# Performance work log

Hardware: AMD Instinct MI355X
Metric: run time of the kernel (lower is better)

## Reference

```python
import jax, jax.numpy as jnp
import numpy as np

B, C, H, W = 8, 3, 720, 1280


def setup_inputs() -> dict:
    key = jax.random.key(0)
    k0, k1 = jax.random.split(key)
    im0 = jax.random.normal(k0, (B, C, H, W), dtype=jnp.float32)
    flow = jax.random.normal(k1, (B, H, W, 2), dtype=jnp.float32)
    return {"im0": im0, "flow": flow}


def reference(im0, flow):
    # Bilinear forward warp (interpolation_mode == 0).
    b, c, h, w = im0.shape
    gy, gx = jnp.meshgrid(jnp.arange(h, dtype=flow.dtype),
                          jnp.arange(w, dtype=flow.dtype), indexing="ij")
    x = gx[None] + flow[..., 0]  # [B,H,W] destination x
    y = gy[None] + flow[..., 1]  # [B,H,W] destination y

    x0 = jnp.floor(x)
    y0 = jnp.floor(y)
    wx1 = x - x0   # weight for x0+1
    wx0 = 1.0 - wx1
    wy1 = y - y0
    wy0 = 1.0 - wy1

    # source values: [B*H*W, C]
    vals = im0.transpose(0, 2, 3, 1).reshape(b * h * w, c)
    boff = (jnp.arange(b, dtype=jnp.int32) * (h * w))[:, None, None]
    out = jnp.zeros((b * h * w, c), dtype=im0.dtype)

    corners = ((x0, y0, wx0 * wy0),
               (x0 + 1.0, y0, wx1 * wy0),
               (x0, y0 + 1.0, wx0 * wy1),
               (x0 + 1.0, y0 + 1.0, wx1 * wy1))
    for xc, yc, wc in corners:
        xi = xc.astype(jnp.int32)
        yi = yc.astype(jnp.int32)
        valid = (xi >= 0) & (xi < w) & (yi >= 0) & (yi < h)
        xi = jnp.clip(xi, 0, w - 1)
        yi = jnp.clip(yi, 0, h - 1)
        idx = (boff + yi * w + xi).reshape(-1)           # [B*H*W]
        wt = jnp.where(valid, wc, 0.0).reshape(-1, 1)    # [B*H*W,1]
        out = out.at[idx].add(wt * vals)
    return out.reshape(b, h, w, c).transpose(0, 3, 1, 2)
```

## Files before the change

kernel.cpp:

```cpp
#include <hip/hip_runtime.h>
#include <hip/hip_fp16.h>

#define BB 8
#define CC 3
#define HH 720
#define WW 1280
#define PLANE (HH*WW)
#define NPIX (BB*HH*WW)

#define PXX 64
#define PYY 8
#define RAD 3
#define NBX (WW/PXX)
#define NBY (HH/PYY)
#define NBLK (BB*NBY*NBX)
#define WINX (PXX+2*RAD)
#define WINY (PYY+2*RAD)
#define NWIN (WINX*WINY)
#define CX 65
#define CY (PYY+1)
#define NCELL (CX*CY)
#define DEPTH 4
#define THREADS 512
#define NBATCH 2
#define OVF_CAP 64

#define OFF_FXY 0
#define OFF_V01 (NCELL*DEPTH)
#define OFF_V2  (2*NCELL*DEPTH)
#define OFF_CNT (2*NCELL*DEPTH + NCELL*DEPTH/2)
#define OFF_LOVF (OFF_CNT + NCELL)
#define LDS_DW  (OFF_LOVF + 1)

static __device__ __forceinline__ float h2f_lo(unsigned int u) {
    return __half2float(__ushort_as_half((unsigned short)(u & 0xffffu)));
}
static __device__ __forceinline__ float h2f_hi(unsigned int u) {
    return __half2float(__ushort_as_half((unsigned short)(u >> 16)));
}

__global__ __launch_bounds__(THREADS) void fw_gather(
    const float* __restrict__ im0,
    const float* __restrict__ flow,
    float* __restrict__ out,
    unsigned int* __restrict__ cnt_g,
    float* __restrict__ ovf_rec)
{
    __shared__ __align__(16) unsigned int lds[LDS_DW];
    unsigned int* FXY = lds + OFF_FXY;
    unsigned int* V01 = lds + OFF_V01;
    unsigned short* V2h = (unsigned short*)(lds + OFF_V2);
    unsigned int* CNT = lds + OFF_CNT;
    unsigned int* LOVF = lds + OFF_LOVF;

    const int phys = blockIdx.x;
    const int virt = (phys & 7) * (NBLK / 8) + (phys >> 3);
    const int b  = virt / (NBX * NBY);
    int r2 = virt - b * (NBX * NBY);
    const int by = r2 / NBX;
    const int bx = r2 - by * NBX;
    const int X0 = bx * PXX, Y0 = by * PYY;
    const int tid = threadIdx.x;

    float2 fv[NBATCH];
    float pv0[NBATCH], pv1[NBATCH], pv2[NBATCH];
    int pgx[NBATCH], pgy[NBATCH];
    bool pok[NBATCH];
#pragma unroll
    for (int t = 0; t < NBATCH; ++t) {
        int i = tid + t * THREADS;
        int wy = i / WINX;
        int wx = i - wy * WINX;
        int gx = X0 - RAD + wx;
        int gy = Y0 - RAD + wy;
        pok[t] = (i < NWIN) & (gx >= 0) & (gx < WW) & (gy >= 0) & (gy < HH);
        pgx[t] = gx; pgy[t] = gy;
        int cgx = min(max(gx, 0), WW - 1);
        int cgy = min(max(gy, 0), HH - 1);
        fv[t] = reinterpret_cast<const float2*>(flow)[(b * HH + cgy) * WW + cgx];
        int src = b * CC * PLANE + cgy * WW + cgx;
        pv0[t] = im0[src];
        pv1[t] = im0[src + PLANE];
        pv2[t] = im0[src + 2 * PLANE];
    }

    uint4* lds4 = reinterpret_cast<uint4*>(lds);
    for (int i = tid; i < LDS_DW / 4; i += THREADS)
        lds4[i] = make_uint4(0u, 0u, 0u, 0u);
    __syncthreads();

#pragma unroll
    for (int t = 0; t < NBATCH; ++t) {
        if (!pok[t]) continue;
        float2 f = fv[t];
        int gx = pgx[t], gy = pgy[t];
        bool reg = (f.x >= -(float)RAD) & (f.x < (float)RAD)
                 & (f.y >= -(float)RAD) & (f.y < (float)RAD);
        if (reg) {
            float x = (float)gx + f.x;
            float y = (float)gy + f.y;
            float x0f = floorf(x), y0f = floorf(y);
            int cx = (int)x0f - (X0 - 1);
            int cy = (int)y0f - (Y0 - 1);
            if (cx >= 0 && cx < CX && cy >= 0 && cy < CY) {
                float fx = x - x0f, fy = y - y0f;
                int cell = cy * CX + cx;
                unsigned int slot = atomicAdd(&CNT[cell], 1u);
                if (slot < DEPTH) {
                    int o = cell * DEPTH + slot;
                    FXY[o] = (unsigned int)__half_as_ushort(__float2half(fx))
                           | ((unsigned int)__half_as_ushort(__float2half(fy)) << 16);
                    V01[o] = (unsigned int)__half_as_ushort(__float2half(pv0[t]))
                           | ((unsigned int)__half_as_ushort(__float2half(pv1[t])) << 16);
                    V2h[o] = __half_as_ushort(__float2half(pv2[t]));
                } else {
                    unsigned int s2 = atomicAdd(LOVF, 1u);
                    if (s2 < OVF_CAP) {
                        float* q = ovf_rec + ((size_t)phys * OVF_CAP + s2) * 6;
                        q[0] = __int_as_float(b | (bx << 4) | (by << 9) | (1 << 16));
                        q[1] = x; q[2] = y;
                        q[3] = pv0[t]; q[4] = pv1[t]; q[5] = pv2[t];
                    }
                }
            }
        } else {
            int wx = gx - (X0 - RAD);
            int wy = gy - (Y0 - RAD);
            if (wx >= RAD && wx < RAD + PXX && wy >= RAD && wy < RAD + PYY) {
                unsigned int s2 = atomicAdd(LOVF, 1u);
                if (s2 < OVF_CAP) {
                    float* q = ovf_rec + ((size_t)phys * OVF_CAP + s2) * 6;
                    q[0] = __int_as_float(b | (bx << 4) | (by << 9));
                    q[1] = (float)gx + f.x; q[2] = (float)gy + f.y;
                    q[3] = pv0[t]; q[4] = pv1[t]; q[5] = pv2[t];
                }
            }
        }
    }
    __syncthreads();

    if (tid == 0) cnt_g[phys] = min(*LOVF, (unsigned int)OVF_CAP);

    const int lane = tid & 63;
    const int wrow = tid >> 6;
    const int X = X0 + lane;
    const int Y = Y0 + wrow;

    float a0 = 0.f, a1 = 0.f, a2 = 0.f;

#pragma unroll
    for (int r = 0; r < 2; ++r) {
        const int cy = wrow + r;
#pragma unroll
        for (int side = 0; side < 2; ++side) {
            const int cell = (cy * CX + lane + side) * DEPTH;
            uint4 fxy4 = *reinterpret_cast<const uint4*>(&FXY[cell]);
            uint4 v014 = *reinterpret_cast<const uint4*>(&V01[cell]);
            ushort4 v24 = *reinterpret_cast<const ushort4*>(&V2h[cell]);
            unsigned int fxys[4] = {fxy4.x, fxy4.y, fxy4.z, fxy4.w};
            unsigned int v01s[4] = {v014.x, v014.y, v014.z, v014.w};
            unsigned short v2s[4] = {v24.x, v24.y, v24.z, v24.w};
#pragma unroll
            for (int k = 0; k < DEPTH; ++k) {
                float fx = h2f_lo(fxys[k]);
                float fy = h2f_hi(fxys[k]);
                float wx  = side ? (1.0f - fx) : fx;
                float wyv = r    ? (1.0f - fy) : fy;
                float wt = wx * wyv;
                a0 += wt * h2f_lo(v01s[k]);
                a1 += wt * h2f_hi(v01s[k]);
                a2 += wt * __half2float(__ushort_as_half(v2s[k]));
            }
        }
    }

    size_t o = (size_t)(b * CC) * PLANE + (size_t)Y * WW + X;
    out[o] = a0;
    out[o + PLANE] = a1;
    out[o + 2 * PLANE] = a2;
}

__global__ __launch_bounds__(256) void fw_overflow(
    const unsigned int* __restrict__ cnt_g,
    const float* __restrict__ ovf_rec,
    float* __restrict__ out)
{
    int i = blockIdx.x * 256 + threadIdx.x;
    if (i >= NBLK * OVF_CAP) return;
    int blk  = i / OVF_CAP;
    int slot = i - blk * OVF_CAP;
    if ((unsigned int)slot >= cnt_g[blk]) return;

    const float* q = ovf_rec + (size_t)i * 6;
    unsigned int meta = __float_as_uint(q[0]);
    int b   = meta & 0xf;
    int rx0 = ((meta >> 4) & 0x1f) * PXX;
    int ry0 = ((meta >> 9) & 0x7f) * PYY;
    int typ = (meta >> 16) & 1;
    float x = q[1], y = q[2];
    float v0 = q[3], v1 = q[4], v2 = q[5];
    float x0f = floorf(x), y0f = floorf(y);
    int x0 = (int)x0f, y0 = (int)y0f;
    float wx1 = x - x0f, wx0 = 1.0f - wx1;
    float wy1 = y - y0f, wy0 = 1.0f - wy1;
#pragma unroll
    for (int dy = 0; dy < 2; ++dy) {
        int yi = y0 + dy;
        float wy = dy ? wy1 : wy0;
#pragma unroll
        for (int dx = 0; dx < 2; ++dx) {
            int xi = x0 + dx;
            bool valid = (xi >= 0) && (xi < WW) && (yi >= 0) && (yi < HH);
            if (typ)
                valid = valid && (xi >= rx0) && (xi < rx0 + PXX)
                              && (yi >= ry0) && (yi < ry0 + PYY);
            if (valid) {
                float wt = wy * (dx ? wx1 : wx0);
                int o = b * CC * PLANE + yi * WW + xi;
                unsafeAtomicAdd(&out[o],             wt * v0);
                unsafeAtomicAdd(&out[o + PLANE],     wt * v1);
                unsafeAtomicAdd(&out[o + 2 * PLANE], wt * v2);
            }
        }
    }
}

__global__ __launch_bounds__(256) void fw_naive(
    const float* __restrict__ im0,
    const float* __restrict__ flow,
    float* __restrict__ out)
{
    int idx = blockIdx.x * blockDim.x + threadIdx.x;
    if (idx >= NPIX) return;
    int w = idx % WW;
    int t = idx / WW;
    int h = t % HH;
    int b = t / HH;
    float2 f = reinterpret_cast<const float2*>(flow)[idx];
    float x = (float)w + f.x, y = (float)h + f.y;
    float x0f = floorf(x), y0f = floorf(y);
    int x0 = (int)x0f, y0 = (int)y0f;
    float wx1 = x - x0f, wx0 = 1.0f - wx1;
    float wy1 = y - y0f, wy0 = 1.0f - wy1;
    int src = (b * CC * HH + h) * WW + w;
    float v0 = im0[src], v1 = im0[src + PLANE], v2 = im0[src + 2 * PLANE];
#pragma unroll
    for (int dy = 0; dy < 2; ++dy) {
        int yi = y0 + dy;
        if (yi < 0 || yi >= HH) continue;
        float wy = dy ? wy1 : wy0;
#pragma unroll
        for (int dx = 0; dx < 2; ++dx) {
            int xi = x0 + dx;
            if (xi < 0 || xi >= WW) continue;
            float wt = wy * (dx ? wx1 : wx0);
            int o = (b * CC) * PLANE + yi * WW + xi;
            unsafeAtomicAdd(&out[o],             wt * v0);
            unsafeAtomicAdd(&out[o + PLANE],     wt * v1);
            unsafeAtomicAdd(&out[o + 2 * PLANE], wt * v2);
        }
    }
}

extern "C" void kernel_launch(void* const* d_in, const int* in_sizes, int n_in,
                              void* d_out, int out_size, void* d_ws, size_t ws_size,
                              hipStream_t stream)
{
    const float* im0  = (const float*)d_in[0];
    const float* flow = (const float*)d_in[1];
    float* out = (float*)d_out;

    const size_t cnt_bytes = (size_t)NBLK * 4;
    const size_t rec_bytes = (size_t)NBLK * OVF_CAP * 24;
    if (ws_size >= cnt_bytes + rec_bytes) {
        unsigned int* cnt = (unsigned int*)d_ws;
        float* rec = (float*)((char*)d_ws + cnt_bytes);

        fw_gather<<<NBLK, THREADS, 0, stream>>>(im0, flow, out, cnt, rec);
        fw_overflow<<<(NBLK * OVF_CAP + 255) / 256, 256, 0, stream>>>(cnt, rec, out);
    } else {
        hipMemsetAsync(out, 0, (size_t)out_size * sizeof(float), stream);
        fw_naive<<<(NPIX + 255) / 256, 256, 0, stream>>>(im0, flow, out);
    }
}
```

Before: 90.67 us.

## Double tile height and compute two output pixels per thread with shared cells

Tile height grows from 8 to 16 rows, which shrinks the relative halo overhead of the window loads and the LDS bin setup. Each thread now produces two horizontally adjacent output pixels, so the middle column of cells is read once for both, and results go out as float2 stores. The change also adds an occupancy hint to launch bounds and guards the partial last load batch. The cost is more registers per thread and a larger LDS footprint, which could limit occupancy.

```diff
diff --git a/kernel.cpp b/kernel.cpp
--- a/kernel.cpp
+++ b/kernel.cpp
@@ -9,7 +9,7 @@
 #define NPIX (BB*HH*WW)
 
 #define PXX 64
-#define PYY 8
+#define PYY 16
 #define RAD 3
 #define NBX (WW/PXX)
 #define NBY (HH/PYY)
@@ -22,7 +22,7 @@
 #define NCELL (CX*CY)
 #define DEPTH 4
 #define THREADS 512
-#define NBATCH 2
+#define NBATCH 4
 #define OVF_CAP 64
 
 #define OFF_FXY 0
@@ -39,7 +39,7 @@
     return __half2float(__ushort_as_half((unsigned short)(u >> 16)));
 }
 
-__global__ __launch_bounds__(THREADS) void fw_gather(
+__global__ __launch_bounds__(THREADS, 6) void fw_gather(
     const float* __restrict__ im0,
     const float* __restrict__ flow,
     float* __restrict__ out,
@@ -75,13 +75,18 @@
         int gy = Y0 - RAD + wy;
         pok[t] = (i < NWIN) & (gx >= 0) & (gx < WW) & (gy >= 0) & (gy < HH);
         pgx[t] = gx; pgy[t] = gy;
-        int cgx = min(max(gx, 0), WW - 1);
-        int cgy = min(max(gy, 0), HH - 1);
-        fv[t] = reinterpret_cast<const float2*>(flow)[(b * HH + cgy) * WW + cgx];
-        int src = b * CC * PLANE + cgy * WW + cgx;
-        pv0[t] = im0[src];
-        pv1[t] = im0[src + PLANE];
-        pv2[t] = im0[src + 2 * PLANE];
+        if (t < NBATCH - 1 || i < NWIN) {
+            int cgx = min(max(gx, 0), WW - 1);
+            int cgy = min(max(gy, 0), HH - 1);
+            fv[t] = reinterpret_cast<const float2*>(flow)[(b * HH + cgy) * WW + cgx];
+            int src = b * CC * PLANE + cgy * WW + cgx;
+            pv0[t] = im0[src];
+            pv1[t] = im0[src + PLANE];
+            pv2[t] = im0[src + 2 * PLANE];
+        } else {
+            fv[t] = make_float2(0.f, 0.f);
+            pv0[t] = 0.f; pv1[t] = 0.f; pv2[t] = 0.f;
+        }
     }
 
     uint4* lds4 = reinterpret_cast<uint4*>(lds);
@@ -141,19 +146,20 @@
 
     if (tid == 0) cnt_g[phys] = min(*LOVF, (unsigned int)OVF_CAP);
 
-    const int lane = tid & 63;
-    const int wrow = tid >> 6;
-    const int X = X0 + lane;
+    const int pcol = tid & 31;
+    const int wrow = tid >> 5;
+    const int X = X0 + 2 * pcol;
     const int Y = Y0 + wrow;
 
-    float a0 = 0.f, a1 = 0.f, a2 = 0.f;
+    float aA0 = 0.f, aA1 = 0.f, aA2 = 0.f;
+    float aB0 = 0.f, aB1 = 0.f, aB2 = 0.f;
 
 #pragma unroll
     for (int r = 0; r < 2; ++r) {
         const int cy = wrow + r;
 #pragma unroll
-        for (int side = 0; side < 2; ++side) {
-            const int cell = (cy * CX + lane + side) * DEPTH;
+        for (int t = 0; t < 3; ++t) {
+            const int cell = (cy * CX + 2 * pcol + t) * DEPTH;
             uint4 fxy4 = *reinterpret_cast<const uint4*>(&FXY[cell]);
             uint4 v014 = *reinterpret_cast<const uint4*>(&V01[cell]);
             ushort4 v24 = *reinterpret_cast<const ushort4*>(&V2h[cell]);
@@ -164,20 +170,30 @@
             for (int k = 0; k < DEPTH; ++k) {
                 float fx = h2f_lo(fxys[k]);
                 float fy = h2f_hi(fxys[k]);
-                float wx  = side ? (1.0f - fx) : fx;
-                float wyv = r    ? (1.0f - fy) : fy;
-                float wt = wx * wyv;
-                a0 += wt * h2f_lo(v01s[k]);
-                a1 += wt * h2f_hi(v01s[k]);
-                a2 += wt * __half2float(__ushort_as_half(v2s[k]));
+                float wyv = r ? (1.0f - fy) : fy;
+                float v0 = h2f_lo(v01s[k]);
+                float v1 = h2f_hi(v01s[k]);
+                float v2 = __half2float(__ushort_as_half(v2s[k]));
+                if (t == 0) {
+                    float wt = fx * wyv;
+                    aA0 += wt * v0; aA1 += wt * v1; aA2 += wt * v2;
+                } else if (t == 1) {
+                    float wtA = (1.0f - fx) * wyv;
+                    float wtB = fx * wyv;
+                    aA0 += wtA * v0; aA1 += wtA * v1; aA2 += wtA * v2;
+                    aB0 += wtB * v0; aB1 += wtB * v1; aB2 += wtB * v2;
+                } else {
+                    float wt = (1.0f - fx) * wyv;
+                    aB0 += wt * v0; aB1 += wt * v1; aB2 += wt * v2;
+                }
             }
         }
     }
 
     size_t o = (size_t)(b * CC) * PLANE + (size_t)Y * WW + X;
-    out[o] = a0;
-    out[o + PLANE] = a1;
-    out[o + 2 * PLANE] = a2;
+    *reinterpret_cast<float2*>(&out[o])             = make_float2(aA0, aB0);
+    *reinterpret_cast<float2*>(&out[o + PLANE])     = make_float2(aA1, aB1);
+    *reinterpret_cast<float2*>(&out[o + 2 * PLANE]) = make_float2(aA2, aB2);
 }
 
 __global__ __launch_bounds__(256) void fw_overflow(
```

After: 114.6 us. 26.4% more time.

## Store precomputed corner weights per cell and accumulate with packed fp16 dot2

Applied to the files above, without the earlier changes.

The scatter phase now computes all four bilinear corner weights at insertion time and stores them, with the three channel values, in a single 56-byte cell record in shared memory. Previously it stored the fractional offsets and separate value arrays. The gather phase reads one weight pair set and the value pairs per cell, then accumulates with v_dot2 fp16 instructions instead of per-entry half-to-float conversions and multiplies. This moves weight arithmetic off the gather path and cuts instruction count, at the cost of more LDS writes per insertion and weights rounded to fp16 before multiplying. The overflow capacity is also halved, which reduces the record buffer.

```diff
diff --git a/kernel.cpp b/kernel.cpp
--- a/kernel.cpp
+++ b/kernel.cpp
@@ -23,21 +23,27 @@
 #define DEPTH 4
 #define THREADS 512
 #define NBATCH 2
-#define OVF_CAP 64
-
-#define OFF_FXY 0
-#define OFF_V01 (NCELL*DEPTH)
-#define OFF_V2  (2*NCELL*DEPTH)
-#define OFF_CNT (2*NCELL*DEPTH + NCELL*DEPTH/2)
+#define OVF_CAP 32
+
+#define CELLB 56
+#define OFF_CNT (NCELL*14)
 #define OFF_LOVF (OFF_CNT + NCELL)
-#define LDS_DW  (OFF_LOVF + 1)
-
-static __device__ __forceinline__ float h2f_lo(unsigned int u) {
-    return __half2float(__ushort_as_half((unsigned short)(u & 0xffffu)));
-}
-static __device__ __forceinline__ float h2f_hi(unsigned int u) {
-    return __half2float(__ushort_as_half((unsigned short)(u >> 16)));
-}
+#define LDS_DW  (OFF_LOVF + 2)
+
+typedef _Float16 hf2_t __attribute__((ext_vector_type(2)));
+
+static __device__ __forceinline__ hf2_t as_h2(unsigned int u) {
+    union { unsigned int u; hf2_t h; } c; c.u = u; return c.h;
+}
+
+#if defined(__has_builtin) && __has_builtin(__builtin_amdgcn_fdot2)
+#define DOT2(w, v, acc) __builtin_amdgcn_fdot2((w), (v), (acc), false)
+#else
+static __device__ __forceinline__ float dot2_fallback(hf2_t w, hf2_t v, float acc) {
+    return acc + (float)w.x * (float)v.x + (float)w.y * (float)v.y;
+}
+#define DOT2(w, v, acc) dot2_fallback((w), (v), (acc))
+#endif
 
 __global__ __launch_bounds__(THREADS) void fw_gather(
     const float* __restrict__ im0,
@@ -47,9 +53,6 @@
     float* __restrict__ ovf_rec)
 {
     __shared__ __align__(16) unsigned int lds[LDS_DW];
-    unsigned int* FXY = lds + OFF_FXY;
-    unsigned int* V01 = lds + OFF_V01;
-    unsigned short* V2h = (unsigned short*)(lds + OFF_V2);
     unsigned int* CNT = lds + OFF_CNT;
     unsigned int* LOVF = lds + OFF_LOVF;
 
@@ -85,7 +88,7 @@
     }
 
     uint4* lds4 = reinterpret_cast<uint4*>(lds);
-    for (int i = tid; i < LDS_DW / 4; i += THREADS)
+    for (int i = tid; i < (LDS_DW + 3) / 4; i += THREADS)
         lds4[i] = make_uint4(0u, 0u, 0u, 0u);
     __syncthreads();
 
@@ -107,12 +110,16 @@
                 int cell = cy * CX + cx;
                 unsigned int slot = atomicAdd(&CNT[cell], 1u);
                 if (slot < DEPTH) {
-                    int o = cell * DEPTH + slot;
-                    FXY[o] = (unsigned int)__half_as_ushort(__float2half(fx))
-                           | ((unsigned int)__half_as_ushort(__float2half(fy)) << 16);
-                    V01[o] = (unsigned int)__half_as_ushort(__float2half(pv0[t]))
-                           | ((unsigned int)__half_as_ushort(__float2half(pv1[t])) << 16);
-                    V2h[o] = __half_as_ushort(__float2half(pv2[t]));
+                    float gx1 = 1.0f - fx, gy1 = 1.0f - fy;
+                    unsigned short* cu =
+                        (unsigned short*)((char*)lds + cell * CELLB);
+                    cu[0 * 4 + slot]  = __half_as_ushort(__float2half(gx1 * gy1));
+                    cu[1 * 4 + slot]  = __half_as_ushort(__float2half(fx  * gy1));
+                    cu[2 * 4 + slot]  = __half_as_ushort(__float2half(gx1 * fy));
+                    cu[3 * 4 + slot]  = __half_as_ushort(__float2half(fx  * fy));
+                    cu[16 + slot]     = __half_as_ushort(__float2half(pv0[t]));
+                    cu[20 + slot]     = __half_as_ushort(__float2half(pv1[t]));
+                    cu[24 + slot]     = __half_as_ushort(__float2half(pv2[t]));
                 } else {
                     unsigned int s2 = atomicAdd(LOVF, 1u);
                     if (s2 < OVF_CAP) {
@@ -153,24 +160,19 @@
         const int cy = wrow + r;
 #pragma unroll
         for (int side = 0; side < 2; ++side) {
-            const int cell = (cy * CX + lane + side) * DEPTH;
-            uint4 fxy4 = *reinterpret_cast<const uint4*>(&FXY[cell]);
-            uint4 v014 = *reinterpret_cast<const uint4*>(&V01[cell]);
-            ushort4 v24 = *reinterpret_cast<const ushort4*>(&V2h[cell]);
-            unsigned int fxys[4] = {fxy4.x, fxy4.y, fxy4.z, fxy4.w};
-            unsigned int v01s[4] = {v014.x, v014.y, v014.z, v014.w};
-            unsigned short v2s[4] = {v24.x, v24.y, v24.z, v24.w};
-#pragma unroll
-            for (int k = 0; k < DEPTH; ++k) {
-                float fx = h2f_lo(fxys[k]);
-                float fy = h2f_hi(fxys[k]);
-                float wx  = side ? (1.0f - fx) : fx;
-                float wyv = r    ? (1.0f - fy) : fy;
-                float wt = wx * wyv;
-                a0 += wt * h2f_lo(v01s[k]);
-                a1 += wt * h2f_hi(v01s[k]);
-                a2 += wt * __half2float(__ushort_as_half(v2s[k]));
-            }
+            const int cell = cy * CX + lane + side;
+            const char* cbase = (const char*)lds + cell * CELLB;
+            const int c = (1 - r) * 2 + (1 - side);
+            uint2 w  = *reinterpret_cast<const uint2*>(cbase + c * 8);
+            uint2 v0 = *reinterpret_cast<const uint2*>(cbase + 32);
+            uint2 v1 = *reinterpret_cast<const uint2*>(cbase + 40);
+            uint2 v2 = *reinterpret_cast<const uint2*>(cbase + 48);
+            a0 = DOT2(as_h2(w.x), as_h2(v0.x), a0);
+            a0 = DOT2(as_h2(w.y), as_h2(v0.y), a0);
+            a1 = DOT2(as_h2(w.x), as_h2(v1.x), a1);
+            a1 = DOT2(as_h2(w.y), as_h2(v1.y), a1);
+            a2 = DOT2(as_h2(w.x), as_h2(v2.x), a2);
+            a2 = DOT2(as_h2(w.y), as_h2(v2.y), a2);
         }
     }
 
```

New measurement: 89.11 us, median of 2. No clear change (-1.7%).
